# Optimization experiments

Measured on AMD Instinct MI355X. Metric: run time of the kernel, lower is better.

## Reference

```python
import jax, jax.numpy as jnp
import numpy as np

K = 10  # topk classes


def setup_inputs() -> dict:
    key = jax.random.key(0)
    ks = jax.random.split(key, 12)
    B, DF, M, C, V, DW, DT = 64, 768, 26, 3129, 10000, 300, 1024
    s = lambda k, sh, scale: jax.random.normal(k, sh, dtype=jnp.float32) * scale
    return {
        "ftm": s(ks[0], (B, DF, M, M), 1.0),
        "logits": s(ks[1], (B, C), 1.0),
        "labels": jax.random.randint(ks[2], (B,), 0, C, dtype=jnp.int32),
        "indices_table": jax.random.randint(ks[3], (C, 4), 0, V, dtype=jnp.int32),
        "word2vec": s(ks[4], (V, DW), 1.0),
        "W_emb": s(ks[5], (DW, DT), 1.0 / np.sqrt(DW)),
        "b_emb": jnp.zeros((DT,), jnp.float32),
        "W_cls": s(ks[6], (DT, DT), 1.0 / np.sqrt(DT)),
        "b_cls": jnp.zeros((DT,), jnp.float32),
        "W_v": s(ks[7], (DF, DT), 1.0 / np.sqrt(DF)),
        "b_v": jnp.zeros((DT,), jnp.float32),
        "W_bap": s(ks[8], (DT, DT), 1.0 / np.sqrt(DT)),
        "b_bap": jnp.zeros((DT,), jnp.float32),
        "W_fc": s(ks[9], (DT, K), 1.0 / np.sqrt(DT)),
        "b_fc": jnp.zeros((K,), jnp.float32),
    }


def reference(ftm, logits, labels, indices_table, word2vec,
              W_emb, b_emb, W_cls, b_cls, W_v, b_v, W_bap, b_bap, W_fc, b_fc):
    B, DF = ftm.shape[0], ftm.shape[1]
    C = logits.shape[1]
    # dispatch: topk classes, gather their word indices, embed
    _, topk_idx = jax.lax.top_k(logits, K)                  # [B, K]
    topk_cls = indices_table[topk_idx]                      # [B, K, 4]
    emb = word2vec[topk_cls].mean(axis=2)                   # [B, K, 300] (ClassEmbedding pooling)
    cls_emb = jax.nn.relu(emb @ W_emb + b_emb)              # [B, K, 1024]
    # SAC_BAP (dropouts in eval mode = identity)
    cls_emb = jax.nn.relu(cls_emb @ W_cls + b_cls)          # [B, K, 1024]
    f = ftm.reshape(B, DF, -1).transpose(0, 2, 1)           # [B, F, 768], F = m*m
    v = jax.nn.relu(f @ W_v + b_v)                          # [B, F, 1024]
    att_w_b_sfx = jnp.einsum('bfd,bkd->bfk', v, cls_emb)    # [B, F, K]
    att_w = jax.nn.softmax(att_w_b_sfx, axis=1)             # softmax over positions
    bap = jnp.einsum('bfd,bfk,bkd->bd', v, att_w, cls_emb)  # [B, 1024]
    bap = jax.nn.relu(bap @ W_bap + b_bap)                  # bap_emb_FC
    bap_logits = bap @ W_fc + b_fc                          # fc_new 1x1 conv -> [B, K]
    # combine: scatter topk logits into the full class space
    um = jnp.zeros((B, C), dtype=bap_logits.dtype)
    um = um.at[jnp.arange(B)[:, None], topk_idx].set(bap_logits)
    return um
```

## Files before the change

kernel.cpp:

```cpp
#include <hip/hip_runtime.h>
#include <hip/hip_bf16.h>

#define B_   64
#define C_   3129
#define K_   10
#define DF_  768
#define F_   676
#define DW_  300
#define DWP_ 320
#define DT_  1024
#define NSEG 4
#define FSEG 169

typedef __attribute__((ext_vector_type(8))) short short8;
typedef __attribute__((ext_vector_type(4))) float floatx4;

__device__ __forceinline__ void gload_lds16(const void* g, void* l) {
    __builtin_amdgcn_global_load_lds(
        (const __attribute__((address_space(1))) void*)g,
        (__attribute__((address_space(3))) void*)l, 16, 0, 0);
}

__global__ void topk_kernel(const float* __restrict__ logits,
                            int* __restrict__ topk_idx) {
    __shared__ float vals[C_];
    __shared__ float red_v[256];
    __shared__ int   red_i[256];
    int b = blockIdx.x;
    int tid = threadIdx.x;
    for (int i = tid; i < C_; i += 256) vals[i] = logits[(size_t)b * C_ + i];
    __syncthreads();
    for (int sel = 0; sel < K_; ++sel) {
        float bv = -INFINITY; int bi = 0x7fffffff;
        for (int i = tid; i < C_; i += 256) {
            float v = vals[i];
            if (v > bv) { bv = v; bi = i; }
        }
        red_v[tid] = bv; red_i[tid] = bi;
        __syncthreads();
        for (int s = 128; s > 0; s >>= 1) {
            if (tid < s) {
                float ov = red_v[tid + s]; int oi = red_i[tid + s];
                if (ov > red_v[tid] || (ov == red_v[tid] && oi < red_i[tid])) {
                    red_v[tid] = ov; red_i[tid] = oi;
                }
            }
            __syncthreads();
        }
        if (tid == 0) {
            topk_idx[b * K_ + sel] = red_i[0];
            vals[red_i[0]] = -INFINITY;
        }
        __syncthreads();
    }
}

__global__ void emb_kernel(const int* __restrict__ topk_idx,
                           const int* __restrict__ indices_table,
                           const float* __restrict__ word2vec,
                           __hip_bfloat16* __restrict__ emb) {
    int idx = blockIdx.x * blockDim.x + threadIdx.x;
    if (idx >= B_ * K_ * DWP_) return;
    int j  = idx % DWP_;
    int bk = idx / DWP_;
    float s = 0.f;
    if (j < DW_) {
        int cls = topk_idx[bk];
        const int* tbl = indices_table + (size_t)cls * 4;
        #pragma unroll
        for (int i = 0; i < 4; ++i) s += word2vec[(size_t)tbl[i] * DW_ + j];
        s *= 0.25f;
    }
    emb[idx] = (__hip_bfloat16)s;
}

__device__ __forceinline__ void tp_body(const float* __restrict__ s,
                                        __hip_bfloat16* __restrict__ d,
                                        int R, int Cc, int Rp, int c0, int r0) {
    __shared__ float tile[64][65];
    int t = threadIdx.x;
    int cl = (t & 15) * 4;
    int rl = t >> 4;
    #pragma unroll
    for (int i = 0; i < 4; ++i) {
        int r = rl + i * 16;
        float4 v = make_float4(0.f, 0.f, 0.f, 0.f);
        if (r0 + r < R && c0 + cl < Cc)
            v = *(const float4*)(s + (size_t)(r0 + r) * Cc + c0 + cl);
        tile[r][cl + 0] = v.x; tile[r][cl + 1] = v.y;
        tile[r][cl + 2] = v.z; tile[r][cl + 3] = v.w;
    }
    __syncthreads();
    int cw = t >> 2;
    int r4 = (t & 3) * 16;
    if (c0 + cw < Cc) {
        __align__(16) __hip_bfloat16 buf[16];
        #pragma unroll
        for (int j = 0; j < 16; ++j) buf[j] = (__hip_bfloat16)tile[r4 + j][cw];
        float4* dp = (float4*)(d + (size_t)(c0 + cw) * Rp + r0 + r4);
        dp[0] = *(float4*)&buf[0];
        dp[1] = *(float4*)&buf[8];
    }
}

__global__ __launch_bounds__(256)
void transpose_ftm(const float* __restrict__ src, __hip_bfloat16* __restrict__ dst) {
    tp_body(src + (size_t)blockIdx.z * DF_ * F_,
            dst + (size_t)blockIdx.z * F_ * DF_,
            DF_, F_, DF_, blockIdx.x * 64, blockIdx.y * 64);
}

__global__ __launch_bounds__(256)
void transpose_weights(const float* __restrict__ Wemb, __hip_bfloat16* __restrict__ WembT,
                       const float* __restrict__ Wcls, __hip_bfloat16* __restrict__ WclsT,
                       const float* __restrict__ Wv,   __hip_bfloat16* __restrict__ WvT,
                       const float* __restrict__ Wbap, __hip_bfloat16* __restrict__ WbapT) {
    int id = blockIdx.x;
    const float* s; __hip_bfloat16* d; int R, Rp;
    if (id < 80)       { s = Wemb; d = WembT; R = DW_;  Rp = DWP_; }
    else if (id < 336) { s = Wcls; d = WclsT; R = DT_;  Rp = DT_;  id -= 80;  }
    else if (id < 528) { s = Wv;   d = WvT;   R = DF_;  Rp = DF_;  id -= 336; }
    else               { s = Wbap; d = WbapT; R = DT_;  Rp = DT_;  id -= 528; }
    int bx = id & 15;
    int by = id >> 4;
    tp_body(s, d, R, DT_, Rp, bx * 64, by * 64);
}

template <int RELU, int OUTBF>
__global__ __launch_bounds__(256)
void gemm_mfma(const __hip_bfloat16* __restrict__ A,
               const __hip_bfloat16* __restrict__ Bt,
               const float* __restrict__ bias,
               void* __restrict__ Cout, int M, int N, int Kp) {
    __shared__ __align__(16) char smem[34816];
    __hip_bfloat16* As = (__hip_bfloat16*)smem;
    __hip_bfloat16* Bs = As + 128 * 64;
    int tid = threadIdx.x;
    int wave = tid >> 6, lane = tid & 63;
    int quad = lane >> 4, l16 = lane & 15;
    int wm = (wave & 1) * 64, wn = (wave >> 1) * 64;
    int n0 = blockIdx.x * 128;
    int m0 = blockIdx.y * 128;

    floatx4 acc[4][4];
    #pragma unroll
    for (int i = 0; i < 4; ++i)
        #pragma unroll
        for (int j = 0; j < 4; ++j)
            acc[i][j] = (floatx4){0.f, 0.f, 0.f, 0.f};

    int rsub = lane >> 3;
    int gchunk = (lane & 7) ^ rsub;

    int arow[4], brow[4];
    #pragma unroll
    for (int i = 0; i < 4; ++i) {
        arow[i] = wm + i * 16 + l16;
        brow[i] = wn + i * 16 + l16;
    }

    for (int k0 = 0; k0 < Kp; k0 += 64) {
        #pragma unroll
        for (int c = 0; c < 4; ++c) {
            int grp = wave * 4 + c;
            int row = grp * 8 + rsub;
            int ra = m0 + row; if (ra >= M) ra = M - 1;
            gload_lds16(A + (size_t)ra * Kp + k0 + gchunk * 8, As + grp * 512);
            gload_lds16(Bt + (size_t)(n0 + row) * Kp + k0 + gchunk * 8, Bs + grp * 512);
        }
        __syncthreads();
        #pragma unroll
        for (int ks = 0; ks < 2; ++ks) {
            short8 af[4], bf[4];
            #pragma unroll
            for (int mi = 0; mi < 4; ++mi)
                af[mi] = *(const short8*)&As[arow[mi] * 64 +
                            ((((ks << 2) | quad) ^ (arow[mi] & 7)) << 3)];
            #pragma unroll
            for (int ni = 0; ni < 4; ++ni)
                bf[ni] = *(const short8*)&Bs[brow[ni] * 64 +
                            ((((ks << 2) | quad) ^ (brow[ni] & 7)) << 3)];
            #pragma unroll
            for (int mi = 0; mi < 4; ++mi)
                #pragma unroll
                for (int ni = 0; ni < 4; ++ni)
                    acc[mi][ni] = __builtin_amdgcn_mfma_f32_16x16x32_bf16(
                        af[mi], bf[ni], acc[mi][ni], 0, 0, 0);
        }
        __syncthreads();
    }

    float bn[4];
    #pragma unroll
    for (int ni = 0; ni < 4; ++ni) bn[ni] = bias[n0 + wn + ni * 16 + l16];

    if (OUTBF) {
        __hip_bfloat16* Cs = (__hip_bfloat16*)smem;
        #pragma unroll
        for (int mi = 0; mi < 4; ++mi)
            #pragma unroll
            for (int rr = 0; rr < 4; ++rr) {
                int row = wm + mi * 16 + quad * 4 + rr;
                #pragma unroll
                for (int ni = 0; ni < 4; ++ni) {
                    float val = acc[mi][ni][rr] + bn[ni];
                    if (RELU) val = fmaxf(val, 0.f);
                    Cs[row * 136 + wn + ni * 16 + l16] = (__hip_bfloat16)val;
                }
            }
        __syncthreads();
        #pragma unroll
        for (int j = 0; j < 8; ++j) {
            int ch = tid + 256 * j;
            int row = ch >> 4, c16 = ch & 15;
            int r = m0 + row;
            float4 val = *(const float4*)&Cs[row * 136 + c16 * 8];
            if (r < M)
                *(float4*)((__hip_bfloat16*)Cout + (size_t)r * N + n0 + c16 * 8) = val;
        }
    } else {
        #pragma unroll
        for (int mi = 0; mi < 4; ++mi)
            #pragma unroll
            for (int rr = 0; rr < 4; ++rr) {
                int r = m0 + wm + mi * 16 + quad * 4 + rr;
                if (r < M) {
                    #pragma unroll
                    for (int ni = 0; ni < 4; ++ni) {
                        float val = acc[mi][ni][rr] + bn[ni];
                        if (RELU) val = fmaxf(val, 0.f);
                        ((float*)Cout)[(size_t)r * N + n0 + wn + ni * 16 + l16] = val;
                    }
                }
            }
    }
}

__global__ __launch_bounds__(256)
void attn_s_kernel(const __hip_bfloat16* __restrict__ v_buf,
                   const __hip_bfloat16* __restrict__ cls,
                   float* __restrict__ s_buf, int b0) {
    int tid = threadIdx.x;
    int wave = tid >> 6, lane = tid & 63;
    int bc = blockIdx.y;
    int f0 = blockIdx.x * 8 + wave * 2;
    int fa = f0 < F_ ? f0 : F_ - 1;
    int fb = (f0 + 1) < F_ ? f0 + 1 : F_ - 1;
    union U { float4 f4; __hip_bfloat16 h[8]; };
    const float4* va = (const float4*)(v_buf + ((size_t)(bc * F_ + fa)) * DT_ + lane * 16);
    const float4* vb = (const float4*)(v_buf + ((size_t)(bc * F_ + fb)) * DT_ + lane * 16);
    U a0, a1, b0u, b1u;
    a0.f4 = va[0]; a1.f4 = va[1];
    b0u.f4 = vb[0]; b1u.f4 = vb[1];
    float av[16], bv[16];
    #pragma unroll
    for (int i = 0; i < 8; ++i) {
        av[i] = (float)a0.h[i]; av[8 + i] = (float)a1.h[i];
        bv[i] = (float)b0u.h[i]; bv[8 + i] = (float)b1u.h[i];
    }
    const __hip_bfloat16* cp = cls + ((size_t)(b0 + bc) * K_) * DT_ + lane * 16;
    #pragma unroll
    for (int k = 0; k < K_; ++k) {
        const float4* c4 = (const float4*)(cp + (size_t)k * DT_);
        U c0u, c1u; c0u.f4 = c4[0]; c1u.f4 = c4[1];
        float da = 0.f, db = 0.f;
        #pragma unroll
        for (int i = 0; i < 8; ++i) {
            float cl0 = (float)c0u.h[i], cl1 = (float)c1u.h[i];
            da += av[i] * cl0 + av[8 + i] * cl1;
            db += bv[i] * cl0 + bv[8 + i] * cl1;
        }
        #pragma unroll
        for (int off = 32; off > 0; off >>= 1) {
            da += __shfl_down(da, off);
            db += __shfl_down(db, off);
        }
        if (lane == 0) {
            if (f0 < F_)     s_buf[((size_t)(bc * F_) + f0) * K_ + k] = da;
            if (f0 + 1 < F_) s_buf[((size_t)(bc * F_) + f0 + 1) * K_ + k] = db;
        }
    }
}

__global__ __launch_bounds__(64)
void softmax_stats(const float* __restrict__ s_buf, float2* __restrict__ ml,
                   int b0) {
    int k = blockIdx.x, bc = blockIdx.y, lane = threadIdx.x;
    const float* sp = s_buf + (size_t)bc * F_ * K_ + k;
    float m = -INFINITY;
    for (int f = lane; f < F_; f += 64) m = fmaxf(m, sp[(size_t)f * K_]);
    #pragma unroll
    for (int off = 32; off > 0; off >>= 1) m = fmaxf(m, __shfl_xor(m, off));
    float l = 0.f;
    for (int f = lane; f < F_; f += 64) l += __expf(sp[(size_t)f * K_] - m);
    #pragma unroll
    for (int off = 32; off > 0; off >>= 1) l += __shfl_xor(l, off);
    if (lane == 0) ml[(size_t)(b0 + bc) * K_ + k] = make_float2(m, 1.f / l);
}

__global__ __launch_bounds__(256)
void o_bap_partial(const __hip_bfloat16* __restrict__ v_buf,
                   const float* __restrict__ s_buf,
                   const float2* __restrict__ ml,
                   const __hip_bfloat16* __restrict__ cls,
                   float* __restrict__ pp, int b0) {
    int bc = blockIdx.x, seg = blockIdx.y;
    int b = b0 + bc;
    int t = threadIdx.x;
    int f0 = seg * FSEG;
    __shared__ float wbuf[FSEG * K_];
    __shared__ float mk[K_], rlk[K_];
    if (t < K_) {
        float2 v = ml[(size_t)b * K_ + t];
        mk[t] = v.x; rlk[t] = v.y;
    }
    __syncthreads();
    for (int j = t; j < FSEG * K_; j += 256) {
        int k = j % K_;
        float sv = s_buf[((size_t)bc * F_ + f0) * K_ + j];
        wbuf[j] = __expf(sv - mk[k]) * rlk[k];
    }
    __syncthreads();
    int d0 = t * 4;
    float acc[K_][4] = {};
    const __hip_bfloat16* vp = v_buf + ((size_t)bc * F_ + f0) * DT_ + d0;
    for (int f = 0; f < FSEG; ++f) {
        union { float2 f2; __hip_bfloat16 h[4]; } u;
        u.f2 = *(const float2*)(vp + (size_t)f * DT_);
        float vv[4];
        #pragma unroll
        for (int i = 0; i < 4; ++i) vv[i] = (float)u.h[i];
        const float* wk = &wbuf[f * K_];
        #pragma unroll
        for (int k = 0; k < K_; ++k)
            #pragma unroll
            for (int i = 0; i < 4; ++i) acc[k][i] += wk[k] * vv[i];
    }
    union { float2 f2; __hip_bfloat16 h[4]; } cu;
    float outv[4] = {};
    #pragma unroll
    for (int k = 0; k < K_; ++k) {
        cu.f2 = *(const float2*)(cls + ((size_t)b * K_ + k) * DT_ + d0);
        #pragma unroll
        for (int i = 0; i < 4; ++i) outv[i] += acc[k][i] * (float)cu.h[i];
    }
    float* pd = pp + ((size_t)seg * B_ + b) * DT_ + d0;
    *(float4*)pd = *(float4*)outv;
}

__global__ void bap_combine(const float* __restrict__ pp,
                            __hip_bfloat16* __restrict__ bap) {
    int idx = blockIdx.x * 256 + threadIdx.x;
    float s = pp[idx] + pp[idx + B_ * DT_] + pp[idx + 2 * B_ * DT_]
            + pp[idx + 3 * B_ * DT_];
    bap[idx] = (__hip_bfloat16)s;
}

__global__ void final_kernel(const float* __restrict__ y,
                             const float* __restrict__ Wfc,
                             const float* __restrict__ bfc,
                             const int* __restrict__ topk_idx,
                             float* __restrict__ out) {
    int b = blockIdx.x, tid = threadIdx.x;
    int lane = tid & 63, wave = tid >> 6;
    float pk[K_] = {};
    for (int d = tid; d < DT_; d += 256) {
        float yv = y[(size_t)b * DT_ + d];
        #pragma unroll
        for (int k = 0; k < K_; ++k) pk[k] += yv * Wfc[(size_t)d * K_ + k];
    }
    __shared__ float wsum[4][K_];
    #pragma unroll
    for (int k = 0; k < K_; ++k) {
        float a = pk[k];
        #pragma unroll
        for (int off = 32; off > 0; off >>= 1) a += __shfl_down(a, off);
        if (lane == 0) wsum[wave][k] = a;
    }
    __syncthreads();
    if (tid < K_) {
        float lg = wsum[0][tid] + wsum[1][tid] + wsum[2][tid] + wsum[3][tid] + bfc[tid];
        out[(size_t)b * C_ + topk_idx[b * K_ + tid]] = lg;
    }
}

extern "C" void kernel_launch(void* const* d_in, const int* in_sizes, int n_in,
                              void* d_out, int out_size, void* d_ws, size_t ws_size,
                              hipStream_t stream) {
    const float* ftm           = (const float*)d_in[0];
    const float* logits        = (const float*)d_in[1];
    const int*   indices_table = (const int*)d_in[3];
    const float* word2vec      = (const float*)d_in[4];
    const float* W_emb         = (const float*)d_in[5];
    const float* b_emb         = (const float*)d_in[6];
    const float* W_cls         = (const float*)d_in[7];
    const float* b_cls         = (const float*)d_in[8];
    const float* W_v           = (const float*)d_in[9];
    const float* b_v           = (const float*)d_in[10];
    const float* W_bap         = (const float*)d_in[11];
    const float* b_bap         = (const float*)d_in[12];
    const float* W_fc          = (const float*)d_in[13];
    const float* b_fc          = (const float*)d_in[14];
    float* out = (float*)d_out;

    char* ws = (char*)d_ws;
    size_t off = 0;
    auto alloc = [&](size_t bytes) -> void* {
        void* p = ws + off;
        off = (off + bytes + 255) & ~(size_t)255;
        return p;
    };
    int*            topk_idx = (int*)           alloc((size_t)B_ * K_ * 4);
    __hip_bfloat16* emb_bf   = (__hip_bfloat16*)alloc((size_t)B_ * K_ * DWP_ * 2);
    __hip_bfloat16* cls1     = (__hip_bfloat16*)alloc((size_t)B_ * K_ * DT_ * 2);
    __hip_bfloat16* cls2     = (__hip_bfloat16*)alloc((size_t)B_ * K_ * DT_ * 2);
    __hip_bfloat16* Wemb_t   = (__hip_bfloat16*)alloc((size_t)DT_ * DWP_ * 2);
    __hip_bfloat16* Wcls_t   = (__hip_bfloat16*)alloc((size_t)DT_ * DT_ * 2);
    __hip_bfloat16* Wv_t     = (__hip_bfloat16*)alloc((size_t)DT_ * DF_ * 2);
    __hip_bfloat16* Wbap_t   = (__hip_bfloat16*)alloc((size_t)DT_ * DT_ * 2);
    float*          s_buf    = (float*)         alloc((size_t)B_ * F_ * K_ * 4);
    float2*         ml       = (float2*)        alloc((size_t)B_ * K_ * 8);
    float*          pp       = (float*)         alloc((size_t)NSEG * B_ * DT_ * 4);
    __hip_bfloat16* bap_bf   = (__hip_bfloat16*)alloc((size_t)B_ * DT_ * 2);
    float*          yb       = (float*)         alloc((size_t)B_ * DT_ * 4);

    size_t per_b = (size_t)F_ * DF_ * 2 + (size_t)F_ * DT_ * 2;
    size_t avail = (ws_size > off + 8192) ? ws_size - off - 8192 : 0;
    int nb = (int)(avail / per_b);
    if (nb > B_) nb = B_;
    if (nb < 1) nb = 1;
    __hip_bfloat16* ftm_t = (__hip_bfloat16*)alloc((size_t)nb * F_ * DF_ * 2);
    __hip_bfloat16* v_buf = (__hip_bfloat16*)alloc((size_t)nb * F_ * DT_ * 2);

    hipMemsetAsync(d_out, 0, (size_t)out_size * sizeof(float), stream);

    topk_kernel<<<B_, 256, 0, stream>>>(logits, topk_idx);
    emb_kernel<<<(B_ * K_ * DWP_ + 255) / 256, 256, 0, stream>>>(
        topk_idx, indices_table, word2vec, emb_bf);

    transpose_weights<<<784, 256, 0, stream>>>(
        W_emb, Wemb_t, W_cls, Wcls_t, W_v, Wv_t, W_bap, Wbap_t);

    gemm_mfma<1, 1><<<dim3(DT_ / 128, (B_ * K_ + 127) / 128), 256, 0, stream>>>(
        emb_bf, Wemb_t, b_emb, cls1, B_ * K_, DT_, DWP_);
    gemm_mfma<1, 1><<<dim3(DT_ / 128, (B_ * K_ + 127) / 128), 256, 0, stream>>>(
        cls1, Wcls_t, b_cls, cls2, B_ * K_, DT_, DT_);

    for (int b0 = 0; b0 < B_; b0 += nb) {
        int cb = min(nb, B_ - b0);
        transpose_ftm<<<dim3((F_ + 63) / 64, DF_ / 64, cb), 256, 0, stream>>>(
            ftm + (size_t)b0 * DF_ * F_, ftm_t);
        int M = cb * F_;
        gemm_mfma<1, 1><<<dim3(DT_ / 128, (M + 127) / 128), 256, 0, stream>>>(
            ftm_t, Wv_t, b_v, v_buf, M, DT_, DF_);
        float* s_c = s_buf + (size_t)b0 * F_ * K_;
        attn_s_kernel<<<dim3((F_ + 7) / 8, cb), 256, 0, stream>>>(
            v_buf, cls2, s_c, b0);
        softmax_stats<<<dim3(K_, cb), 64, 0, stream>>>(s_c, ml, b0);
        o_bap_partial<<<dim3(cb, NSEG), 256, 0, stream>>>(
            v_buf, s_c, ml, cls2, pp, b0);
    }
    bap_combine<<<B_ * DT_ / 256, 256, 0, stream>>>(pp, bap_bf);

    gemm_mfma<1, 0><<<dim3(DT_ / 128, 1), 256, 0, stream>>>(
        bap_bf, Wbap_t, b_bap, yb, B_, DT_, DT_);
    final_kernel<<<B_, 256, 0, stream>>>(yb, W_fc, b_fc, topk_idx, out);
}
```

Measured before the change: 527.6 us.

## Fuse topk+embedding, merge transposes, inline softmax stats, swizzle V GEMM grid

```diff
diff --git a/kernel.cpp b/kernel.cpp
--- a/kernel.cpp
+++ b/kernel.cpp
@@ -21,11 +21,15 @@
         (__attribute__((address_space(3))) void*)l, 16, 0, 0);
 }
 
-__global__ void topk_kernel(const float* __restrict__ logits,
-                            int* __restrict__ topk_idx) {
+__global__ void topk_emb_kernel(const float* __restrict__ logits,
+                                const int* __restrict__ indices_table,
+                                const float* __restrict__ word2vec,
+                                int* __restrict__ topk_idx,
+                                __hip_bfloat16* __restrict__ emb) {
     __shared__ float vals[C_];
     __shared__ float red_v[256];
     __shared__ int   red_i[256];
+    __shared__ int   sel_idx[K_];
     int b = blockIdx.x;
     int tid = threadIdx.x;
     for (int i = tid; i < C_; i += 256) vals[i] = logits[(size_t)b * C_ + i];
@@ -49,29 +53,24 @@
         }
         if (tid == 0) {
             topk_idx[b * K_ + sel] = red_i[0];
+            sel_idx[sel] = red_i[0];
             vals[red_i[0]] = -INFINITY;
         }
         __syncthreads();
     }
-}
-
-__global__ void emb_kernel(const int* __restrict__ topk_idx,
-                           const int* __restrict__ indices_table,
-                           const float* __restrict__ word2vec,
-                           __hip_bfloat16* __restrict__ emb) {
-    int idx = blockIdx.x * blockDim.x + threadIdx.x;
-    if (idx >= B_ * K_ * DWP_) return;
-    int j  = idx % DWP_;
-    int bk = idx / DWP_;
-    float s = 0.f;
-    if (j < DW_) {
-        int cls = topk_idx[bk];
-        const int* tbl = indices_table + (size_t)cls * 4;
-        #pragma unroll
-        for (int i = 0; i < 4; ++i) s += word2vec[(size_t)tbl[i] * DW_ + j];
-        s *= 0.25f;
-    }
-    emb[idx] = (__hip_bfloat16)s;
+    for (int idx = tid; idx < K_ * DWP_; idx += 256) {
+        int j = idx % DWP_;
+        int k = idx / DWP_;
+        float s = 0.f;
+        if (j < DW_) {
+            int cls = sel_idx[k];
+            const int* tbl = indices_table + (size_t)cls * 4;
+            #pragma unroll
+            for (int i = 0; i < 4; ++i) s += word2vec[(size_t)tbl[i] * DW_ + j];
+            s *= 0.25f;
+        }
+        emb[((size_t)b * K_ + k) * DWP_ + j] = (__hip_bfloat16)s;
+    }
 }
 
 __device__ __forceinline__ void tp_body(const float* __restrict__ s,
@@ -103,19 +102,11 @@
     }
 }
 
-__global__ __launch_bounds__(256)
-void transpose_ftm(const float* __restrict__ src, __hip_bfloat16* __restrict__ dst) {
-    tp_body(src + (size_t)blockIdx.z * DF_ * F_,
-            dst + (size_t)blockIdx.z * F_ * DF_,
-            DF_, F_, DF_, blockIdx.x * 64, blockIdx.y * 64);
-}
-
-__global__ __launch_bounds__(256)
-void transpose_weights(const float* __restrict__ Wemb, __hip_bfloat16* __restrict__ WembT,
-                       const float* __restrict__ Wcls, __hip_bfloat16* __restrict__ WclsT,
-                       const float* __restrict__ Wv,   __hip_bfloat16* __restrict__ WvT,
-                       const float* __restrict__ Wbap, __hip_bfloat16* __restrict__ WbapT) {
-    int id = blockIdx.x;
+__device__ __forceinline__ void tp_weights(int id,
+        const float* Wemb, __hip_bfloat16* WembT,
+        const float* Wcls, __hip_bfloat16* WclsT,
+        const float* Wv,   __hip_bfloat16* WvT,
+        const float* Wbap, __hip_bfloat16* WbapT) {
     const float* s; __hip_bfloat16* d; int R, Rp;
     if (id < 80)       { s = Wemb; d = WembT; R = DW_;  Rp = DWP_; }
     else if (id < 336) { s = Wcls; d = WclsT; R = DT_;  Rp = DT_;  id -= 80;  }
@@ -126,12 +117,57 @@
     tp_body(s, d, R, DT_, Rp, bx * 64, by * 64);
 }
 
-template <int RELU, int OUTBF>
+__global__ __launch_bounds__(256)
+void transpose_weights(const float* __restrict__ Wemb, __hip_bfloat16* __restrict__ WembT,
+                       const float* __restrict__ Wcls, __hip_bfloat16* __restrict__ WclsT,
+                       const float* __restrict__ Wv,   __hip_bfloat16* __restrict__ WvT,
+                       const float* __restrict__ Wbap, __hip_bfloat16* __restrict__ WbapT) {
+    tp_weights(blockIdx.x, Wemb, WembT, Wcls, WclsT, Wv, WvT, Wbap, WbapT);
+}
+
+__global__ __launch_bounds__(256)
+void transpose_ftm(const float* __restrict__ src, __hip_bfloat16* __restrict__ dst) {
+    tp_body(src + (size_t)blockIdx.z * DF_ * F_,
+            dst + (size_t)blockIdx.z * F_ * DF_,
+            DF_, F_, DF_, blockIdx.x * 64, blockIdx.y * 64);
+}
+
+__global__ __launch_bounds__(256)
+void transpose_all(const float* __restrict__ Wemb, __hip_bfloat16* __restrict__ WembT,
+                   const float* __restrict__ Wcls, __hip_bfloat16* __restrict__ WclsT,
+                   const float* __restrict__ Wv,   __hip_bfloat16* __restrict__ WvT,
+                   const float* __restrict__ Wbap, __hip_bfloat16* __restrict__ WbapT,
+                   const float* __restrict__ ftm,  __hip_bfloat16* __restrict__ ftmT) {
+    int id = blockIdx.x;
+    if (id < 784) {
+        tp_weights(id, Wemb, WembT, Wcls, WclsT, Wv, WvT, Wbap, WbapT);
+    } else {
+        id -= 784;
+        int z = id / 132, rem = id % 132;
+        int bx = rem % 11, by = rem / 11;
+        tp_body(ftm + (size_t)z * DF_ * F_, ftmT + (size_t)z * F_ * DF_,
+                DF_, F_, DF_, bx * 64, by * 64);
+    }
+}
+
+template <int RELU, int OUTBF, int SWZ>
 __global__ __launch_bounds__(256)
 void gemm_mfma(const __hip_bfloat16* __restrict__ A,
                const __hip_bfloat16* __restrict__ Bt,
                const float* __restrict__ bias,
                void* __restrict__ Cout, int M, int N, int Kp) {
+    int n0, m0;
+    if (SWZ) {
+        int mblocks = (M + 127) >> 7;
+        int slab = gridDim.y >> 3;
+        int m = (blockIdx.y >> 3) + slab * blockIdx.x;
+        if (m >= mblocks) return;
+        n0 = (blockIdx.y & 7) * 128;
+        m0 = m * 128;
+    } else {
+        n0 = blockIdx.x * 128;
+        m0 = blockIdx.y * 128;
+    }
     __shared__ __align__(16) char smem[34816];
     __hip_bfloat16* As = (__hip_bfloat16*)smem;
     __hip_bfloat16* Bs = As + 128 * 64;
@@ -139,8 +175,6 @@
     int wave = tid >> 6, lane = tid & 63;
     int quad = lane >> 4, l16 = lane & 15;
     int wm = (wave & 1) * 64, wn = (wave >> 1) * 64;
-    int n0 = blockIdx.x * 128;
-    int m0 = blockIdx.y * 128;
 
     floatx4 acc[4][4];
     #pragma unroll
@@ -282,39 +316,42 @@
     }
 }
 
-__global__ __launch_bounds__(64)
-void softmax_stats(const float* __restrict__ s_buf, float2* __restrict__ ml,
-                   int b0) {
-    int k = blockIdx.x, bc = blockIdx.y, lane = threadIdx.x;
-    const float* sp = s_buf + (size_t)bc * F_ * K_ + k;
-    float m = -INFINITY;
-    for (int f = lane; f < F_; f += 64) m = fmaxf(m, sp[(size_t)f * K_]);
-    #pragma unroll
-    for (int off = 32; off > 0; off >>= 1) m = fmaxf(m, __shfl_xor(m, off));
-    float l = 0.f;
-    for (int f = lane; f < F_; f += 64) l += __expf(sp[(size_t)f * K_] - m);
-    #pragma unroll
-    for (int off = 32; off > 0; off >>= 1) l += __shfl_xor(l, off);
-    if (lane == 0) ml[(size_t)(b0 + bc) * K_ + k] = make_float2(m, 1.f / l);
-}
-
 __global__ __launch_bounds__(256)
 void o_bap_partial(const __hip_bfloat16* __restrict__ v_buf,
                    const float* __restrict__ s_buf,
-                   const float2* __restrict__ ml,
                    const __hip_bfloat16* __restrict__ cls,
                    float* __restrict__ pp, int b0) {
     int bc = blockIdx.x, seg = blockIdx.y;
     int b = b0 + bc;
     int t = threadIdx.x;
     int f0 = seg * FSEG;
+    __shared__ float sm[16 * 16], sl[16 * 16];
+    __shared__ float mk[K_], rlk[K_];
+    {
+        int k = t & 15, g = t >> 4;
+        float m = -INFINITY, l = 0.f;
+        if (k < K_) {
+            const float* sp = s_buf + (size_t)bc * F_ * K_ + k;
+            for (int f = g; f < F_; f += 16) {
+                float x = sp[(size_t)f * K_];
+                if (x > m) { l = l * __expf(m - x) + 1.f; m = x; }
+                else       { l += __expf(x - m); }
+            }
+            sm[k * 16 + g] = m; sl[k * 16 + g] = l;
+        }
+        __syncthreads();
+        if (t < K_) {
+            float M = -INFINITY, L = 0.f;
+            for (int g2 = 0; g2 < 16; ++g2) {
+                float mi = sm[t * 16 + g2], li = sl[t * 16 + g2];
+                if (mi > M) { L = L * __expf(M - mi) + li; M = mi; }
+                else        { L += li * __expf(mi - M); }
+            }
+            mk[t] = M; rlk[t] = 1.f / L;
+        }
+        __syncthreads();
+    }
     __shared__ float wbuf[FSEG * K_];
-    __shared__ float mk[K_], rlk[K_];
-    if (t < K_) {
-        float2 v = ml[(size_t)b * K_ + t];
-        mk[t] = v.x; rlk[t] = v.y;
-    }
-    __syncthreads();
     for (int j = t; j < FSEG * K_; j += 256) {
         int k = j % K_;
         float sv = s_buf[((size_t)bc * F_ + f0) * K_ + j];
@@ -363,6 +400,7 @@
                              float* __restrict__ out) {
     int b = blockIdx.x, tid = threadIdx.x;
     int lane = tid & 63, wave = tid >> 6;
+    for (int i = tid; i < C_; i += 256) out[(size_t)b * C_ + i] = 0.f;
     float pk[K_] = {};
     for (int d = tid; d < DT_; d += 256) {
         float yv = y[(size_t)b * DT_ + d];
@@ -419,7 +457,6 @@
     __hip_bfloat16* Wv_t     = (__hip_bfloat16*)alloc((size_t)DT_ * DF_ * 2);
     __hip_bfloat16* Wbap_t   = (__hip_bfloat16*)alloc((size_t)DT_ * DT_ * 2);
     float*          s_buf    = (float*)         alloc((size_t)B_ * F_ * K_ * 4);
-    float2*         ml       = (float2*)        alloc((size_t)B_ * K_ * 8);
     float*          pp       = (float*)         alloc((size_t)NSEG * B_ * DT_ * 4);
     __hip_bfloat16* bap_bf   = (__hip_bfloat16*)alloc((size_t)B_ * DT_ * 2);
     float*          yb       = (float*)         alloc((size_t)B_ * DT_ * 4);
@@ -432,37 +469,42 @@
     __hip_bfloat16* ftm_t = (__hip_bfloat16*)alloc((size_t)nb * F_ * DF_ * 2);
     __hip_bfloat16* v_buf = (__hip_bfloat16*)alloc((size_t)nb * F_ * DT_ * 2);
 
-    hipMemsetAsync(d_out, 0, (size_t)out_size * sizeof(float), stream);
-
-    topk_kernel<<<B_, 256, 0, stream>>>(logits, topk_idx);
-    emb_kernel<<<(B_ * K_ * DWP_ + 255) / 256, 256, 0, stream>>>(
-        topk_idx, indices_table, word2vec, emb_bf);
-
-    transpose_weights<<<784, 256, 0, stream>>>(
-        W_emb, Wemb_t, W_cls, Wcls_t, W_v, Wv_t, W_bap, Wbap_t);
-
-    gemm_mfma<1, 1><<<dim3(DT_ / 128, (B_ * K_ + 127) / 128), 256, 0, stream>>>(
+    topk_emb_kernel<<<B_, 256, 0, stream>>>(logits, indices_table, word2vec,
+                                            topk_idx, emb_bf);
+
+    if (nb == B_) {
+        transpose_all<<<784 + B_ * 132, 256, 0, stream>>>(
+            W_emb, Wemb_t, W_cls, Wcls_t, W_v, Wv_t, W_bap, Wbap_t, ftm, ftm_t);
+    } else {
+        transpose_weights<<<784, 256, 0, stream>>>(
+            W_emb, Wemb_t, W_cls, Wcls_t, W_v, Wv_t, W_bap, Wbap_t);
+    }
+
+    gemm_mfma<1, 1, 0><<<dim3(DT_ / 128, 5), 256, 0, stream>>>(
         emb_bf, Wemb_t, b_emb, cls1, B_ * K_, DT_, DWP_);
-    gemm_mfma<1, 1><<<dim3(DT_ / 128, (B_ * K_ + 127) / 128), 256, 0, stream>>>(
+    gemm_mfma<1, 1, 0><<<dim3(DT_ / 128, 5), 256, 0, stream>>>(
         cls1, Wcls_t, b_cls, cls2, B_ * K_, DT_, DT_);
 
     for (int b0 = 0; b0 < B_; b0 += nb) {
         int cb = min(nb, B_ - b0);
-        transpose_ftm<<<dim3((F_ + 63) / 64, DF_ / 64, cb), 256, 0, stream>>>(
-            ftm + (size_t)b0 * DF_ * F_, ftm_t);
+        if (nb != B_) {
+            transpose_ftm<<<dim3(11, 12, cb), 256, 0, stream>>>(
+                ftm + (size_t)b0 * DF_ * F_, ftm_t);
+        }
         int M = cb * F_;
-        gemm_mfma<1, 1><<<dim3(DT_ / 128, (M + 127) / 128), 256, 0, stream>>>(
+        int mblocks = (M + 127) / 128;
+        int mb_pad = (mblocks + 7) & ~7;
+        gemm_mfma<1, 1, 1><<<dim3(8, mb_pad), 256, 0, stream>>>(
             ftm_t, Wv_t, b_v, v_buf, M, DT_, DF_);
         float* s_c = s_buf + (size_t)b0 * F_ * K_;
         attn_s_kernel<<<dim3((F_ + 7) / 8, cb), 256, 0, stream>>>(
             v_buf, cls2, s_c, b0);
-        softmax_stats<<<dim3(K_, cb), 64, 0, stream>>>(s_c, ml, b0);
         o_bap_partial<<<dim3(cb, NSEG), 256, 0, stream>>>(
-            v_buf, s_c, ml, cls2, pp, b0);
+            v_buf, s_c, cls2, pp, b0);
     }
     bap_combine<<<B_ * DT_ / 256, 256, 0, stream>>>(pp, bap_bf);
 
-    gemm_mfma<1, 0><<<dim3(DT_ / 128, 1), 256, 0, stream>>>(
+    gemm_mfma<1, 0, 0><<<dim3(DT_ / 128, 1), 256, 0, stream>>>(
         bap_bf, Wbap_t, b_bap, yb, B_, DT_, DT_);
     final_kernel<<<B_, 256, 0, stream>>>(yb, W_fc, b_fc, topk_idx, out);
 }
```

Measured after the change: 529.6 us. No clear change (+0.4%).
